# Performance work log

Hardware: AMD Instinct MI355X
Metric: run time of the kernel (lower is better)

## Reference

```python
import jax, jax.numpy as jnp
import numpy as np

T, D, K = 16384, 512, 128
NODES = [512, 512]


def _rnn_layer(X, Wx, Wh, bh, h0):
    # X: [T, M1] -> [T, M2]; precompute input projection (parallel part)
    Xp = X @ Wx  # [T, M2]
    def step(h, x):
        h = jax.nn.relu(x + h @ Wh + bh)
        return h, h
    _, out = jax.lax.scan(step, h0[0], Xp)
    return out  # [T, M2]


def setup_inputs() -> dict:
    key = jax.random.key(0)
    ks = jax.random.split(key, 16)
    inp = {"X": jax.random.normal(ks[0], (T, D), dtype=jnp.float32)}
    M1 = D
    for i, M2 in enumerate(NODES):
        s = 1.0 / np.sqrt(M1 + M2)
        inp[f"Wx{i}"] = jax.random.normal(ks[1 + 3 * i], (M1, M2), dtype=jnp.float32) * s
        inp[f"Wh{i}"] = jax.random.normal(ks[2 + 3 * i], (M2, M2), dtype=jnp.float32) * s
        inp[f"bh{i}"] = jnp.zeros((M2,), dtype=jnp.float32)
        inp[f"h0{i}"] = jnp.zeros((1, M2), dtype=jnp.float32)
        M1 = M2
    # nn.Linear(M1, K): weight [K, M1], bias [K]
    lim = 1.0 / np.sqrt(M1)
    inp["W_log"] = jax.random.uniform(ks[10], (K, M1), minval=-lim, maxval=lim, dtype=jnp.float32)
    inp["b_log"] = jax.random.uniform(ks[11], (K,), minval=-lim, maxval=lim, dtype=jnp.float32)
    return inp


def reference(X, Wx0, Wh0, bh0, h00, Wx1, Wh1, bh1, h01, W_log, b_log):
    h = _rnn_layer(X, Wx0, Wh0, bh0, h00)
    h = _rnn_layer(h, Wx1, Wh1, bh1, h01)
    return h @ W_log.T + b_log  # [T, K]
```

## Files before the change

### kernel.cpp

```cpp
#include <hip/hip_runtime.h>
#include <stdint.h>

#define TT 16384
#define DH 512
#define KK 128
#define SENT 0xAAAAAAAAu

__device__ __forceinline__ uint32_t agent_load(const uint32_t* p) {
    return __hip_atomic_load(p, __ATOMIC_RELAXED, __HIP_MEMORY_SCOPE_AGENT);
}
__device__ __forceinline__ void agent_store(uint32_t* p, uint32_t v) {
    __hip_atomic_store(p, v, __ATOMIC_RELAXED, __HIP_MEMORY_SCOPE_AGENT);
}

__global__ __launch_bounds__(256, 1)
void rnn_scan(const float* __restrict__ X,
              const float* __restrict__ Wx0, const float* __restrict__ Wh0,
              const float* __restrict__ bh0, const float* __restrict__ h00,
              const float* __restrict__ Wx1, const float* __restrict__ Wh1,
              const float* __restrict__ bh1, const float* __restrict__ h01,
              float* __restrict__ H0, float* __restrict__ H1)
{
    const int layer = blockIdx.x >> 4;
    const int slice = blockIdx.x & 15;
    const int tid   = threadIdx.x;
    const int o     = tid & 31;
    const int c     = tid >> 5;
    const int og    = slice * 32 + o;

    const float* Wx = layer ? Wx1 : Wx0;
    const float* Wh = layer ? Wh1 : Wh0;
    const float* bh = layer ? bh1 : bh0;
    const float* h0 = layer ? h01 : h00;
    float* Hout = layer ? H1 : H0;

    float wx[64], wh[64];
    #pragma unroll
    for (int j = 0; j < 64; ++j) {
        int i = c * 64 + j;
        wx[j] = Wx[i * DH + og];
        wh[j] = Wh[i * DH + og];
    }
    const float bias = bh[og];

    __shared__ __align__(16) float hbuf[DH];
    __shared__ __align__(16) float xbuf[DH];
    __shared__ float partials[8 * 33];

    hbuf[tid]       = h0[tid];
    hbuf[tid + 256] = h0[tid + 256];

    const uint32_t* Xpoll = (const uint32_t*)H0;
    uint32_t* Hout_u = (uint32_t*)Hout;
    const uint32_t* Hprev_u = (const uint32_t*)Hout;

    float xc0 = 0.f, xc1 = 0.f, xn0 = 0.f, xn1 = 0.f;
    if (layer == 0) {
        xc0 = X[tid];
        xc1 = X[tid + 256];
    }

    for (int t = 0; t < TT; ++t) {
        if (layer == 0) {
            xbuf[tid]       = xc0;
            xbuf[tid + 256] = xc1;
            if (t + 1 < TT) {
                xn0 = X[(t + 1) * DH + tid];
                xn1 = X[(t + 1) * DH + tid + 256];
            }
        } else {
            uint32_t v0, v1;
            do { v0 = agent_load(&Xpoll[t * DH + tid]); }       while (v0 == SENT);
            do { v1 = agent_load(&Xpoll[t * DH + tid + 256]); } while (v1 == SENT);
            xbuf[tid]       = __uint_as_float(v0);
            xbuf[tid + 256] = __uint_as_float(v1);
        }

        uint32_t hv0 = 0, hv1 = 0;
        if (t > 0) {
            hv0 = agent_load(&Hprev_u[(t - 1) * DH + tid]);
            hv1 = agent_load(&Hprev_u[(t - 1) * DH + tid + 256]);
        }

        __syncthreads();

        float acc = 0.f;
        {
            const float4* x4 = (const float4*)&xbuf[c * 64];
            #pragma unroll
            for (int j4 = 0; j4 < 16; ++j4) {
                float4 xv = x4[j4];
                acc += wx[4 * j4 + 0] * xv.x + wx[4 * j4 + 1] * xv.y
                     + wx[4 * j4 + 2] * xv.z + wx[4 * j4 + 3] * xv.w;
            }
        }

        if (t > 0) {
            while (hv0 == SENT) hv0 = agent_load(&Hprev_u[(t - 1) * DH + tid]);
            while (hv1 == SENT) hv1 = agent_load(&Hprev_u[(t - 1) * DH + tid + 256]);
            hbuf[tid]       = __uint_as_float(hv0);
            hbuf[tid + 256] = __uint_as_float(hv1);
        }

        __syncthreads();

        {
            const float4* h4 = (const float4*)&hbuf[c * 64];
            #pragma unroll
            for (int j4 = 0; j4 < 16; ++j4) {
                float4 hv = h4[j4];
                acc += wh[4 * j4 + 0] * hv.x + wh[4 * j4 + 1] * hv.y
                     + wh[4 * j4 + 2] * hv.z + wh[4 * j4 + 3] * hv.w;
            }
        }
        partials[c * 33 + o] = acc;

        __syncthreads();

        if (tid < 32) {
            float v = bias;
            #pragma unroll
            for (int cc = 0; cc < 8; ++cc) v += partials[cc * 33 + tid];
            v = fmaxf(v, 0.f);
            agent_store(&Hout_u[t * DH + og], __float_as_uint(v));
        }

        if (layer == 0) { xc0 = xn0; xc1 = xn1; }
    }
}

__global__ __launch_bounds__(128, 1)
void logits_kernel(const float* __restrict__ H1, const float* __restrict__ Wl,
                   const float* __restrict__ bl, float* __restrict__ out)
{
    const int t0 = blockIdx.x * 8;
    const int k  = threadIdx.x;

    __shared__ __align__(16) float hs[8 * DH];
    for (int idx = k; idx < 8 * DH / 4; idx += 128)
        ((float4*)hs)[idx] = ((const float4*)&H1[(size_t)t0 * DH])[idx];
    __syncthreads();

    float acc[8];
    const float bk = bl[k];
    #pragma unroll
    for (int r = 0; r < 8; ++r) acc[r] = bk;

    const float4* w4 = (const float4*)&Wl[k * DH];
    for (int j = 0; j < DH / 4; ++j) {
        float4 w = w4[j];
        #pragma unroll
        for (int r = 0; r < 8; ++r) {
            float4 h = ((const float4*)&hs[r * DH])[j];
            acc[r] += w.x * h.x + w.y * h.y + w.z * h.z + w.w * h.w;
        }
    }
    #pragma unroll
    for (int r = 0; r < 8; ++r) out[(size_t)(t0 + r) * KK + k] = acc[r];
}

extern "C" void kernel_launch(void* const* d_in, const int* in_sizes, int n_in,
                              void* d_out, int out_size, void* d_ws, size_t ws_size,
                              hipStream_t stream)
{
    const float* X   = (const float*)d_in[0];
    const float* Wx0 = (const float*)d_in[1];
    const float* Wh0 = (const float*)d_in[2];
    const float* bh0 = (const float*)d_in[3];
    const float* h00 = (const float*)d_in[4];
    const float* Wx1 = (const float*)d_in[5];
    const float* Wh1 = (const float*)d_in[6];
    const float* bh1 = (const float*)d_in[7];
    const float* h01 = (const float*)d_in[8];
    const float* Wl  = (const float*)d_in[9];
    const float* bl  = (const float*)d_in[10];
    float* out = (float*)d_out;

    float* H0 = (float*)d_ws;
    float* H1 = H0 + (size_t)TT * DH;

    hipMemsetAsync(d_ws, 0xAA, (size_t)2 * TT * DH * sizeof(float), stream);

    hipLaunchKernelGGL(rnn_scan, dim3(32), dim3(256), 0, stream,
                       X, Wx0, Wh0, bh0, h00, Wx1, Wh1, bh1, h01, H0, H1);
    hipLaunchKernelGGL(logits_kernel, dim3(TT / 8), dim3(128), 0, stream,
                       H1, Wl, bl, out);
}
```

Measured before the change: 24.43 ms.

## Split input projections into parallel GEMM blocks overlapped with recurrence scan

The input projections X@Wx are moved out of the serial scan into separate producer blocks. These compute 32-row chunks as tiled GEMMs and publish per-chunk flags. Recurrent blocks now use 1024 threads covering 128 outputs each, and exchange hidden states through a small parity-tagged ring buffer so no sentinel memset is needed per step. Each step only has to do the h@Wh matvec, at the cost of complex cross-block flag protocols, buffer reuse of H1r as scratch for Xp0, and reliance on co-residency of 64 blocks.

```diff
diff --git a/kernel.cpp b/kernel.cpp
--- a/kernel.cpp
+++ b/kernel.cpp
@@ -5,127 +5,211 @@
 #define DH 512
 #define KK 128
 #define SENT 0xAAAAAAAAu
-
-__device__ __forceinline__ uint32_t agent_load(const uint32_t* p) {
+#define CROWS 32
+#define NCHUNK (TT / CROWS)
+#define NPROJ 56
+#define RSLOT 16
+
+__device__ uint32_t g_ring[2][RSLOT][DH];
+__device__ uint32_t g_flagXp[2][NCHUNK];
+
+static __device__ __forceinline__ uint32_t aload(const uint32_t* p) {
     return __hip_atomic_load(p, __ATOMIC_RELAXED, __HIP_MEMORY_SCOPE_AGENT);
 }
-__device__ __forceinline__ void agent_store(uint32_t* p, uint32_t v) {
+static __device__ __forceinline__ void astore(uint32_t* p, uint32_t v) {
     __hip_atomic_store(p, v, __ATOMIC_RELAXED, __HIP_MEMORY_SCOPE_AGENT);
 }
-
-__global__ __launch_bounds__(256, 1)
-void rnn_scan(const float* __restrict__ X,
-              const float* __restrict__ Wx0, const float* __restrict__ Wh0,
-              const float* __restrict__ bh0, const float* __restrict__ h00,
-              const float* __restrict__ Wx1, const float* __restrict__ Wh1,
-              const float* __restrict__ bh1, const float* __restrict__ h01,
-              float* __restrict__ H0, float* __restrict__ H1)
-{
-    const int layer = blockIdx.x >> 4;
-    const int slice = blockIdx.x & 15;
-    const int tid   = threadIdx.x;
-    const int o     = tid & 31;
-    const int c     = tid >> 5;
-    const int og    = slice * 32 + o;
-
-    const float* Wx = layer ? Wx1 : Wx0;
-    const float* Wh = layer ? Wh1 : Wh0;
-    const float* bh = layer ? bh1 : bh0;
-    const float* h0 = layer ? h01 : h00;
-    float* Hout = layer ? H1 : H0;
-
-    float wx[64], wh[64];
-    #pragma unroll
-    for (int j = 0; j < 64; ++j) {
-        int i = c * 64 + j;
-        wx[j] = Wx[i * DH + og];
-        wh[j] = Wh[i * DH + og];
-    }
-    const float bias = bh[og];
-
-    __shared__ __align__(16) float hbuf[DH];
-    __shared__ __align__(16) float xbuf[DH];
-    __shared__ float partials[8 * 33];
-
-    hbuf[tid]       = h0[tid];
-    hbuf[tid + 256] = h0[tid + 256];
-
-    const uint32_t* Xpoll = (const uint32_t*)H0;
-    uint32_t* Hout_u = (uint32_t*)Hout;
-    const uint32_t* Hprev_u = (const uint32_t*)Hout;
-
-    float xc0 = 0.f, xc1 = 0.f, xn0 = 0.f, xn1 = 0.f;
-    if (layer == 0) {
-        xc0 = X[tid];
-        xc1 = X[tid + 256];
-    }
-
-    for (int t = 0; t < TT; ++t) {
-        if (layer == 0) {
-            xbuf[tid]       = xc0;
-            xbuf[tid + 256] = xc1;
-            if (t + 1 < TT) {
-                xn0 = X[(t + 1) * DH + tid];
-                xn1 = X[(t + 1) * DH + tid + 256];
-            }
+static __device__ __forceinline__ float aloadf(const float* p) {
+    return __uint_as_float(aload((const uint32_t*)p));
+}
+
+__global__ void init_kernel() {
+    const int tid = threadIdx.x;
+    uint32_t* r = &g_ring[0][0][0];
+    for (int i = tid; i < 2 * RSLOT * DH; i += 1024) r[i] = SENT;
+    uint32_t* f = &g_flagXp[0][0];
+    for (int i = tid; i < 2 * NCHUNK; i += 1024) f[i] = SENT;
+}
+
+static __device__ void proj_chunk(const float* __restrict__ W,
+                                  const float* __restrict__ src, int srcMode,
+                                  float* __restrict__ dst, uint32_t* flag, int t0,
+                                  float* inT , float* wt )
+{
+    const int tid = threadIdx.x;
+    #pragma unroll
+    for (int i = 0; i < 16; ++i) {
+        int idx = tid + 1024 * i;
+        int row = idx >> 9;
+        int col = idx & 511;
+        float v;
+        if (srcMode == 0) {
+            v = src[(size_t)t0 * DH + idx];
         } else {
-            uint32_t v0, v1;
-            do { v0 = agent_load(&Xpoll[t * DH + tid]); }       while (v0 == SENT);
-            do { v1 = agent_load(&Xpoll[t * DH + tid + 256]); } while (v1 == SENT);
-            xbuf[tid]       = __uint_as_float(v0);
-            xbuf[tid + 256] = __uint_as_float(v1);
-        }
-
-        uint32_t hv0 = 0, hv1 = 0;
-        if (t > 0) {
-            hv0 = agent_load(&Hprev_u[(t - 1) * DH + tid]);
-            hv1 = agent_load(&Hprev_u[(t - 1) * DH + tid + 256]);
-        }
-
+            const uint32_t* p = (const uint32_t*)src + (size_t)t0 * DH + idx;
+            uint32_t u;
+            while ((u = aload(p)) == SENT) __builtin_amdgcn_s_sleep(1);
+            v = __uint_as_float(u);
+        }
+        inT[col * 36 + row] = v;
+    }
+    __syncthreads();
+
+    const int rg = (tid >> 7) & 7;
+    const int cg = tid & 127;
+    float acc[4][4] = {{0.f}};
+
+    for (int kt = 0; kt < 16; ++kt) {
+        const int k0 = kt * 32;
+        #pragma unroll
+        for (int i = 0; i < 4; ++i) {
+            int f4 = tid + 1024 * i;
+            int wr = f4 >> 7;
+            int wc = (f4 & 127) << 2;
+            *(float4*)&wt[wr * 516 + wc] =
+                *(const float4*)&W[(size_t)(k0 + wr) * DH + wc];
+        }
         __syncthreads();
-
-        float acc = 0.f;
-        {
-            const float4* x4 = (const float4*)&xbuf[c * 64];
-            #pragma unroll
-            for (int j4 = 0; j4 < 16; ++j4) {
-                float4 xv = x4[j4];
-                acc += wx[4 * j4 + 0] * xv.x + wx[4 * j4 + 1] * xv.y
-                     + wx[4 * j4 + 2] * xv.z + wx[4 * j4 + 3] * xv.w;
-            }
-        }
-
-        if (t > 0) {
-            while (hv0 == SENT) hv0 = agent_load(&Hprev_u[(t - 1) * DH + tid]);
-            while (hv1 == SENT) hv1 = agent_load(&Hprev_u[(t - 1) * DH + tid + 256]);
-            hbuf[tid]       = __uint_as_float(hv0);
-            hbuf[tid + 256] = __uint_as_float(hv1);
-        }
-
+        #pragma unroll 8
+        for (int kk = 0; kk < 32; ++kk) {
+            float4 a = *(const float4*)&inT[(k0 + kk) * 36 + (rg << 2)];
+            float4 w = *(const float4*)&wt[kk * 516 + (cg << 2)];
+            acc[0][0] += a.x * w.x; acc[0][1] += a.x * w.y; acc[0][2] += a.x * w.z; acc[0][3] += a.x * w.w;
+            acc[1][0] += a.y * w.x; acc[1][1] += a.y * w.y; acc[1][2] += a.y * w.z; acc[1][3] += a.y * w.w;
+            acc[2][0] += a.z * w.x; acc[2][1] += a.z * w.y; acc[2][2] += a.z * w.z; acc[2][3] += a.z * w.w;
+            acc[3][0] += a.w * w.x; acc[3][1] += a.w * w.y; acc[3][2] += a.w * w.z; acc[3][3] += a.w * w.w;
+        }
         __syncthreads();
-
-        {
-            const float4* h4 = (const float4*)&hbuf[c * 64];
-            #pragma unroll
-            for (int j4 = 0; j4 < 16; ++j4) {
-                float4 hv = h4[j4];
-                acc += wh[4 * j4 + 0] * hv.x + wh[4 * j4 + 1] * hv.y
-                     + wh[4 * j4 + 2] * hv.z + wh[4 * j4 + 3] * hv.w;
-            }
-        }
-        partials[c * 33 + o] = acc;
-
+    }
+    #pragma unroll
+    for (int i = 0; i < 4; ++i)
+        #pragma unroll
+        for (int j = 0; j < 4; ++j)
+            astore((uint32_t*)&dst[(size_t)(t0 + (rg << 2) + i) * DH + (cg << 2) + j],
+                   __float_as_uint(acc[i][j]));
+    __threadfence();
+    __syncthreads();
+    if (tid == 0)
+        __hip_atomic_store(flag, 1u, __ATOMIC_RELEASE, __HIP_MEMORY_SCOPE_AGENT);
+}
+
+__global__ __launch_bounds__(1024, 1)
+void fused(const float* __restrict__ X,
+           const float* __restrict__ Wx0, const float* __restrict__ Wh0,
+           const float* __restrict__ bh0, const float* __restrict__ h00,
+           const float* __restrict__ Wx1, const float* __restrict__ Wh1,
+           const float* __restrict__ bh1, const float* __restrict__ h01,
+           float* H0r, float* H1r)
+{
+    __shared__ __align__(16) float s_hbuf[DH];
+    __shared__ float s_part[8][128];
+    __shared__ __align__(16) float s_inT[DH * 36];
+    __shared__ __align__(16) float s_wt[32 * 516];
+
+    const int bIdx = blockIdx.x;
+    const int m8 = bIdx & 7;
+    const int tid = threadIdx.x;
+
+    if (bIdx < 32 && m8 < 2) {
+        const int L = m8;
+        const int b = bIdx >> 3;
+        const int c = tid >> 7;
+        const int o = tid & 127;
+        const int og = (b << 7) + o;
+
+        const float* Wh  = L ? Wh1 : Wh0;
+        const float* bhv = L ? bh1 : bh0;
+        const float* h0v = L ? h01 : h00;
+        float* Hful      = L ? H1r : H0r;
+        const float* Xp  = L ? H0r : H1r;
+        uint32_t* ring         = &g_ring[L][0][0];
+        uint32_t* flagXp       = &g_flagXp[L][0];
+
+        float wh[64];
+        #pragma unroll
+        for (int j = 0; j < 64; ++j)
+            wh[j] = Wh[(size_t)((c << 6) + j) * DH + og];
+        const float bias = bhv[og];
+
+        const int ptid = (tid + 1024 - ((b << 8) + 256)) & 1023;
+        const bool isPoll = ptid < 384;
+        const int pcol = (ptid < (b << 7)) ? ptid : ptid + 128;
+        const bool isSelf = (c >> 1) == b;
+        const bool isRed = tid < 128;
+
+        if (tid < DH) s_hbuf[tid] = h0v[tid];
+
+        float xp_next = 0.f;
+        int curCh = -1;
+        if (isRed) {
+            while (__hip_atomic_load(&flagXp[0], __ATOMIC_ACQUIRE,
+                                     __HIP_MEMORY_SCOPE_AGENT) != 1u)
+                __builtin_amdgcn_s_sleep(1);
+            curCh = 0;
+            xp_next = aloadf(&Xp[og]);
+        }
         __syncthreads();
 
-        if (tid < 32) {
-            float v = bias;
-            #pragma unroll
-            for (int cc = 0; cc < 8; ++cc) v += partials[cc * 33 + tid];
-            v = fmaxf(v, 0.f);
-            agent_store(&Hout_u[t * DH + og], __float_as_uint(v));
-        }
-
-        if (layer == 0) { xc0 = xn0; xc1 = xn1; }
+        for (int t = 0; t < TT; ++t) {
+            if (t > 0 && isPoll) {
+                const uint32_t par = (uint32_t)((t - 1) >> 4) & 1u;
+                const uint32_t* p = &ring[(((t - 1) & 15) << 9) + pcol];
+                uint32_t v;
+                do { v = aload(p); } while ((v >> 31) != par);
+                s_hbuf[pcol] = __uint_as_float(v & 0x7fffffffu);
+            }
+            float acc = 0.f;
+            if (isSelf | (t == 0)) {
+                const float4* h4 = (const float4*)&s_hbuf[c << 6];
+                #pragma unroll
+                for (int j4 = 0; j4 < 16; ++j4) {
+                    float4 hv = h4[j4];
+                    acc += wh[4*j4+0]*hv.x + wh[4*j4+1]*hv.y
+                         + wh[4*j4+2]*hv.z + wh[4*j4+3]*hv.w;
+                }
+                s_part[c][o] = acc;
+            }
+            __syncthreads();
+            if (!(isSelf | (t == 0))) {
+                const float4* h4 = (const float4*)&s_hbuf[c << 6];
+                #pragma unroll
+                for (int j4 = 0; j4 < 16; ++j4) {
+                    float4 hv = h4[j4];
+                    acc += wh[4*j4+0]*hv.x + wh[4*j4+1]*hv.y
+                         + wh[4*j4+2]*hv.z + wh[4*j4+3]*hv.w;
+                }
+                s_part[c][o] = acc;
+            }
+            __syncthreads();
+            if (isRed) {
+                float v = bias + xp_next;
+                #pragma unroll
+                for (int cc = 0; cc < 8; ++cc) v += s_part[cc][o];
+                v = fmaxf(v, 0.f);
+                const uint32_t hb = __float_as_uint(v);
+                astore(&ring[((t & 15) << 9) + og],
+                       hb | (((uint32_t)(t >> 4) & 1u) << 31));
+                astore((uint32_t*)Hful + (size_t)t * DH + og, hb);
+                s_hbuf[og] = v;
+                if (t + 1 < TT) {
+                    const int ch = (t + 1) >> 5;
+                    if (ch != curCh) {
+                        while (__hip_atomic_load(&flagXp[ch], __ATOMIC_ACQUIRE,
+                                                 __HIP_MEMORY_SCOPE_AGENT) != 1u) {}
+                        curCh = ch;
+                    }
+                    xp_next = aloadf(&Xp[(size_t)(t + 1) * DH + og]);
+                }
+            }
+            __syncthreads();
+        }
+    } else {
+        const int pi = (bIdx < 32) ? (((bIdx >> 3) * 6) + (m8 - 2))
+                                   : (24 + (bIdx - 32));
+        for (int cc = pi; cc < NCHUNK; cc += NPROJ) {
+            proj_chunk(Wx0, X,   0, H1r , &g_flagXp[0][cc], cc * CROWS, s_inT, s_wt);
+            proj_chunk(Wx1, H0r, 1, H0r , &g_flagXp[1][cc], cc * CROWS, s_inT, s_wt);
+        }
     }
 }
 
@@ -134,7 +218,7 @@
                    const float* __restrict__ bl, float* __restrict__ out)
 {
     const int t0 = blockIdx.x * 8;
-    const int k  = threadIdx.x;
+    const int k = threadIdx.x;
 
     __shared__ __align__(16) float hs[8 * DH];
     for (int idx = k; idx < 8 * DH / 4; idx += 128)
@@ -146,7 +230,7 @@
     #pragma unroll
     for (int r = 0; r < 8; ++r) acc[r] = bk;
 
-    const float4* w4 = (const float4*)&Wl[k * DH];
+    const float4* w4 = (const float4*)&Wl[(size_t)k * DH];
     for (int j = 0; j < DH / 4; ++j) {
         float4 w = w4[j];
         #pragma unroll
@@ -176,13 +260,13 @@
     const float* bl  = (const float*)d_in[10];
     float* out = (float*)d_out;
 
-    float* H0 = (float*)d_ws;
-    float* H1 = H0 + (size_t)TT * DH;
-
-    hipMemsetAsync(d_ws, 0xAA, (size_t)2 * TT * DH * sizeof(float), stream);
-
-    hipLaunchKernelGGL(rnn_scan, dim3(32), dim3(256), 0, stream,
-                       X, Wx0, Wh0, bh0, h00, Wx1, Wh1, bh1, h01, H0, H1);
+    float* H0r = (float*)d_ws;
+    float* H1r = H0r + (size_t)TT * DH;
+
+    hipMemsetAsync(d_ws, 0xAA, (size_t)TT * DH * sizeof(float), stream);
+    hipLaunchKernelGGL(init_kernel, dim3(1), dim3(1024), 0, stream);
+    hipLaunchKernelGGL(fused, dim3(64), dim3(1024), 0, stream,
+                       X, Wx0, Wh0, bh0, h00, Wx1, Wh1, bh1, h01, H0r, H1r);
     hipLaunchKernelGGL(logits_kernel, dim3(TT / 8), dim3(128), 0, stream,
-                       H1, Wl, bl, out);
-}
+                       H1r, Wl, bl, out);
+}
```

New measurement: 20.13 ms. -17.6%, faster.
